# Performance work log

Measured on AMD Instinct MI355X. Metric: run time of the kernel, lower is better.

## Reference

```python
import jax, jax.numpy as jnp
import numpy as np
from jax import lax

ANG = 9
MIND, MAXD = -4, 4
EPS = 1e-5


def conv(x, w, stride=1, dilation=1, padding=0, groups=1):
    return lax.conv_general_dilated(
        x, w, (stride, stride), [(padding, padding)] * 2,
        rhs_dilation=(dilation, dilation),
        dimension_numbers=('NCHW', 'OIHW', 'NCHW'),
        feature_group_count=groups)


def bn_relu(x, g, b):
    # training-mode BatchNorm2d (biased batch stats) + ReLU, as in torch default forward
    m = x.mean((0, 2, 3), keepdims=True)
    v = ((x - m) ** 2).mean((0, 2, 3), keepdims=True)
    y = (x - m) * lax.rsqrt(v + EPS) * g.reshape(1, -1, 1, 1) + b.reshape(1, -1, 1, 1)
    return jax.nn.relu(y)


def sai2macpi(x, ang):
    # out[:, :, i*ang+u, j*ang+v] = x[:, :, u*h+i, v*w+j]  (pure strided rearrange)
    b, c, hu, wv = x.shape
    h, w = hu // ang, wv // ang
    x = x.reshape(b, c, ang, h, ang, w)
    return x.transpose(0, 1, 3, 2, 5, 4).reshape(b, c, h * ang, w * ang)


def _shift_idx(n, ang, dil, pad):
    # per-view-block gather indices replicating Unfold(k=ang,dil,pad,stride=ang)->Fold
    idx = jnp.arange(n)[:, None] * ang + jnp.arange(ang)[None, :] * dil - pad  # [n, ang]
    valid = (idx >= 0) & (idx < n * ang)
    return jnp.clip(idx, 0, n * ang - 1).reshape(-1), valid.reshape(-1)


def disp_shift(feat, d, ang):
    b, c, hu, wv = feat.shape
    h, w = hu // ang, wv // ang
    if d < 0:
        dil = -d * ang + 1
        pad = ang * (ang - 1) * (-d) // 2
    elif d == 0:
        dil, pad = 1, 0
    else:
        dil = d * ang - 1
        pad = ang * (ang - 1) * d // 2 - ang + 1
    ih, mh = _shift_idx(h, ang, dil, pad)
    iw, mw = _shift_idx(w, ang, dil, pad)
    out = feat[:, :, ih, :][:, :, :, iw]
    mask = (mh[:, None] & mw[None, :]).astype(feat.dtype)
    return out * mask


def setup_inputs() -> dict:
    key = jax.random.key(0)
    ks = jax.random.split(key, 16)
    b, h, w = 2, 96, 96
    hu, wv = h * ANG, w * ANG
    s = 0.1
    inp = {
        'x': jax.random.normal(ks[0], (b, 1, hu, wv), jnp.float32),
        'fw0': jax.random.normal(ks[1], (7, 1, 3, 3), jnp.float32) * s,
        'fg0': jnp.ones((7,), jnp.float32),
        'fb0': jnp.zeros((7,), jnp.float32),
        'fw': jax.random.normal(ks[2], (6, 7, 7, 3, 3), jnp.float32) * s,
        'fg': jnp.ones((6, 7), jnp.float32),
        'fb': jnp.zeros((6, 7), jnp.float32),
        'bc_w': jax.random.normal(ks[3], (144, 7, 9, 9), jnp.float32) * 0.04,
        'agg0_dw': jax.random.normal(ks[4], (144, 1, 3, 3), jnp.float32) * s,
        'agg0_dg': jnp.ones((144,), jnp.float32),
        'agg0_db': jnp.zeros((144,), jnp.float32),
        'agg0_pw': jax.random.normal(ks[5], (180, 144, 1, 1), jnp.float32) * s,
        'agg0_pg': jnp.ones((180,), jnp.float32),
        'agg0_pb': jnp.zeros((180,), jnp.float32),
        'aggm_dw': jax.random.normal(ks[6], (4, 180, 1, 3, 3), jnp.float32) * s,
        'aggm_dg': jnp.ones((4, 180), jnp.float32),
        'aggm_db': jnp.zeros((4, 180), jnp.float32),
        'aggm_pw': jax.random.normal(ks[7], (4, 180, 180, 1, 1), jnp.float32) * s,
        'aggm_pg': jnp.ones((4, 180), jnp.float32),
        'aggm_pb': jnp.zeros((4, 180), jnp.float32),
        'last_dw': jax.random.normal(ks[8], (180, 1, 3, 3), jnp.float32) * s,
        'last_dg': jnp.ones((180,), jnp.float32),
        'last_db': jnp.zeros((180,), jnp.float32),
        'last_pw': jax.random.normal(ks[9], (9, 180, 1, 1), jnp.float32) * s,
    }
    return inp


def reference(x, fw0, fg0, fb0, fw, fg, fb, bc_w,
              agg0_dw, agg0_dg, agg0_db, agg0_pw, agg0_pg, agg0_pb,
              aggm_dw, aggm_dg, aggm_db, aggm_pw, aggm_pg, aggm_pb,
              last_dw, last_dg, last_db, last_pw):
    # SAI -> MacPI rearrange
    f = sai2macpi(x, ANG)
    f = bn_relu(conv(f, fw0, dilation=ANG, padding=ANG), fg0, fb0)
    for i in range(6):
        f = bn_relu(conv(f, fw[i], dilation=ANG, padding=ANG), fg[i], fb[i])
    # per-disparity Unfold/Fold shift -> concat [b, 9*7, hu, wv]
    vol = jnp.concatenate([disp_shift(f, d, ANG) for d in range(MIND, MAXD + 1)], axis=1)
    # BuildCost: grouped conv, kernel=stride=angRes -> [b, 144, h, w]
    cv = conv(vol, bc_w, stride=ANG, groups=9)
    # aggregation: depthwise-separable blocks
    y = bn_relu(conv(cv, agg0_dw, padding=1, groups=144), agg0_dg, agg0_db)
    y = bn_relu(conv(y, agg0_pw), agg0_pg, agg0_pb)
    for i in range(4):
        y = bn_relu(conv(y, aggm_dw[i], padding=1, groups=180), aggm_dg[i], aggm_db[i])
        y = bn_relu(conv(y, aggm_pw[i]), aggm_pg[i], aggm_pb[i])
    y = bn_relu(conv(y, last_dw, padding=1, groups=180), last_dg, last_db)
    cost = conv(y, last_pw)  # [b, 9, h, w]
    score = jax.nn.softmax(cost, axis=1)
    disps = jnp.arange(MIND, MAXD + 1, dtype=score.dtype).reshape(1, -1, 1, 1)
    return jnp.sum(score * disps, axis=1, keepdims=True)  # [b, 1, h, w]
```

## Files before the change

kernel.cpp:

```cpp
#include <hip/hip_runtime.h>

#define ANG 9
#define HH 96
#define BB 2
#define PLANE_F (81*HH*HH)
#define PLANE_A (HH*HH)
#define NBLK_FEAT 1458
#define INV_NSMALL (1.0f / 18432.0f)

typedef float f4 __attribute__((ext_vector_type(4), aligned(4)));

__device__ __forceinline__ void row3sel(const float* rp, int base, bool j0, bool j95,
                                        float& w0, float& w1, float& w2) {
  f4 v = *(const f4*)(rp + base);
  w0 = j95 ? v.z : v.x;
  w1 = j0 ? v.x : (j95 ? v.w : v.y);
  w2 = j0 ? v.y : v.z;
}

__global__ __launch_bounds__(256) void k_bnfinal(const float* __restrict__ psum,
    const float* __restrict__ psq, const float* __restrict__ g, const float* __restrict__ bbias,
    float* __restrict__ sc, float* __restrict__ sh, int NB, float invN) {
  int c = blockIdx.x, tid = threadIdx.x;
  float s = 0.f, q = 0.f;
  for (int k = tid; k < NB; k += 256) { s += psum[c * NB + k]; q += psq[c * NB + k]; }
  __shared__ float ss[256], qq[256];
  ss[tid] = s; qq[tid] = q;
  __syncthreads();
  for (int st = 128; st > 0; st >>= 1) {
    if (tid < st) { ss[tid] += ss[tid + st]; qq[tid] += qq[tid + st]; }
    __syncthreads();
  }
  if (tid == 0) {
    float mean = ss[0] * invN;
    float var = fmaxf(qq[0] * invN - mean * mean, 0.f);
    float scale = g[c] / sqrtf(var + 1e-5f);
    sc[c] = scale; sh[c] = bbias[c] - mean * scale;
  }
}

__global__ __launch_bounds__(256) void k_wprep(const float* __restrict__ bcw,
    const float* __restrict__ a0pw, const float* __restrict__ ampw, const float* __restrict__ lpw,
    float* __restrict__ wt, float* __restrict__ wpt) {
  int k = blockIdx.x * 256 + threadIdx.x;
  if (k < 81648) {
    int o = k & 15; int rest = k >> 4;
    int r81 = rest % 81; int gc = rest / 81;
    int c = gc % 7, g = gc / 7;
    wt[k] = bcw[((g * 16 + o) * 7 + c) * 81 + r81];
    return;
  }
  int t = k - 81648;
  if (t < 25920) {
    int c = t / 180, o = t % 180;
    wpt[t] = a0pw[o * 144 + c];
  } else if (t < 25920 + 129600) {
    int t2 = t - 25920;
    int m = t2 / 32400, r = t2 % 32400;
    int c = r / 180, o = r % 180;
    wpt[t] = ampw[m * 32400 + o * 180 + c];
  } else if (t < 25920 + 129600 + 1620) {
    int t2 = t - 25920 - 129600;
    int c = t2 / 9, o = t2 % 9;
    wpt[t] = lpw[o * 180 + c];
  }
}

__global__ __launch_bounds__(256, 4) void k_featconv0(const float* __restrict__ x,
    const float* __restrict__ w, float* __restrict__ out,
    float* __restrict__ psum, float* __restrict__ psq) {
  int blk = blockIdx.x, tid = threadIdx.x;
  int view = blk / 9, q = blk % 9;
  int b = view / 81, uv = view % 81;
  int u = uv / 9, v = uv % 9;
  int widx = q * 256 + tid;
  int j = widx % HH, i0 = (widx / HH) * 4;
  bool j0 = (j == 0), j95 = (j == 95);
  int base = j0 ? 0 : (j95 ? 92 : j - 1);
  float me0 = j0 ? 0.f : 1.f, me2 = j95 ? 0.f : 1.f;
  const float* bx = x + (size_t)b * PLANE_F + (u * HH) * 864 + v * HH;
  float win[6][3];
  #pragma unroll
  for (int r6 = 0; r6 < 6; r6++) {
    int ii = i0 + r6 - 1;
    float mi = ((unsigned)ii < 96u) ? 1.f : 0.f;
    int iic = min(max(ii, 0), 95);
    float w0, w1, w2;
    row3sel(bx + iic * 864, base, j0, j95, w0, w1, w2);
    win[r6][0] = w0 * (mi * me0);
    win[r6][1] = w1 * mi;
    win[r6][2] = w2 * (mi * me2);
  }
  float acc[4][7];
  #pragma unroll
  for (int px = 0; px < 4; px++)
    #pragma unroll
    for (int o = 0; o < 7; o++) acc[px][o] = 0.f;
  #pragma unroll
  for (int o = 0; o < 7; o++) {
    const float* wc = w + o * 9;
    #pragma unroll
    for (int ky = 0; ky < 3; ky++)
      #pragma unroll
      for (int kx = 0; kx < 3; kx++) {
        float wv = wc[ky * 3 + kx];
        #pragma unroll
        for (int px = 0; px < 4; px++)
          acc[px][o] = fmaf(win[px + ky][kx], wv, acc[px][o]);
      }
  }
  #pragma unroll
  for (int o = 0; o < 7; o++) {
    float* op = out + ((size_t)(b * 7 + o)) * PLANE_F + uv * PLANE_A + i0 * HH + j;
    #pragma unroll
    for (int px = 0; px < 4; px++) op[px * HH] = acc[px][o];
  }
  float sv[7], qv[7];
  #pragma unroll
  for (int o = 0; o < 7; o++) {
    sv[o] = acc[0][o] + acc[1][o] + acc[2][o] + acc[3][o];
    qv[o] = acc[0][o]*acc[0][o] + acc[1][o]*acc[1][o] + acc[2][o]*acc[2][o] + acc[3][o]*acc[3][o];
  }
  #pragma unroll
  for (int off2 = 32; off2 > 0; off2 >>= 1)
    #pragma unroll
    for (int o = 0; o < 7; o++) { sv[o] += __shfl_down(sv[o], off2); qv[o] += __shfl_down(qv[o], off2); }
  __shared__ float red[4][14];
  int wave = tid >> 6, lane = tid & 63;
  if (lane == 0) {
    #pragma unroll
    for (int o = 0; o < 7; o++) { red[wave][o] = sv[o]; red[wave][7 + o] = qv[o]; }
  }
  __syncthreads();
  if (tid < 14) {
    float t4 = red[0][tid] + red[1][tid] + red[2][tid] + red[3][tid];
    if (tid < 7) psum[tid * NBLK_FEAT + blk] = t4;
    else         psq[(tid - 7) * NBLK_FEAT + blk] = t4;
  }
}

__global__ __launch_bounds__(256, 4) void k_featconv4(const float* __restrict__ in,
    const float* __restrict__ w, const float* __restrict__ sc, const float* __restrict__ sh,
    float* __restrict__ out, float* __restrict__ psum, float* __restrict__ psq) {
  int blk = blockIdx.x, tid = threadIdx.x;
  int view = blk / 9, q = blk % 9;
  int b = view / 81, uv = view % 81;
  int widx = q * 256 + tid;
  int j = widx % HH, i0 = (widx / HH) * 4;
  bool j0 = (j == 0), j95 = (j == 95);
  int base = j0 ? 0 : (j95 ? 92 : j - 1);
  float me0 = j0 ? 0.f : 1.f, me2 = j95 ? 0.f : 1.f;
  float mrow[6]; int roff[6];
  #pragma unroll
  for (int r6 = 0; r6 < 6; r6++) {
    int ii = i0 + r6 - 1;
    mrow[r6] = ((unsigned)ii < 96u) ? 1.f : 0.f;
    roff[r6] = min(max(ii, 0), 95) * HH + base;
  }
  float acc[4][7];
  #pragma unroll
  for (int px = 0; px < 4; px++)
    #pragma unroll
    for (int o = 0; o < 7; o++) acc[px][o] = 0.f;
  const float* ipbase = in + ((size_t)(b * 7)) * PLANE_F + uv * PLANE_A;
  float pre[6][3];
  #pragma unroll
  for (int r6 = 0; r6 < 6; r6++)
    row3sel(ipbase + roff[r6], 0, j0, j95, pre[r6][0], pre[r6][1], pre[r6][2]);
  #pragma unroll 1
  for (int c = 0; c < 7; c++) {
    float s = sc[c], h2 = sh[c];
    float win[6][3];
    #pragma unroll
    for (int r6 = 0; r6 < 6; r6++) {
      win[r6][0] = fmaxf(fmaf(pre[r6][0], s, h2), 0.f) * (mrow[r6] * me0);
      win[r6][1] = fmaxf(fmaf(pre[r6][1], s, h2), 0.f) * mrow[r6];
      win[r6][2] = fmaxf(fmaf(pre[r6][2], s, h2), 0.f) * (mrow[r6] * me2);
    }
    if (c < 6) {
      const float* ipn = ipbase + (size_t)(c + 1) * PLANE_F;
      #pragma unroll
      for (int r6 = 0; r6 < 6; r6++)
        row3sel(ipn + roff[r6], 0, j0, j95, pre[r6][0], pre[r6][1], pre[r6][2]);
    }
    #pragma unroll
    for (int o = 0; o < 7; o++) {
      const float* wc = w + (o * 7 + c) * 9;
      #pragma unroll
      for (int ky = 0; ky < 3; ky++)
        #pragma unroll
        for (int kx = 0; kx < 3; kx++) {
          float wv = wc[ky * 3 + kx];
          #pragma unroll
          for (int px = 0; px < 4; px++)
            acc[px][o] = fmaf(win[px + ky][kx], wv, acc[px][o]);
        }
    }
  }
  #pragma unroll
  for (int o = 0; o < 7; o++) {
    float* op = out + ((size_t)(b * 7 + o)) * PLANE_F + uv * PLANE_A + i0 * HH + j;
    #pragma unroll
    for (int px = 0; px < 4; px++) op[px * HH] = acc[px][o];
  }
  float sv[7], qv[7];
  #pragma unroll
  for (int o = 0; o < 7; o++) {
    sv[o] = acc[0][o] + acc[1][o] + acc[2][o] + acc[3][o];
    qv[o] = acc[0][o]*acc[0][o] + acc[1][o]*acc[1][o] + acc[2][o]*acc[2][o] + acc[3][o]*acc[3][o];
  }
  #pragma unroll
  for (int off2 = 32; off2 > 0; off2 >>= 1)
    #pragma unroll
    for (int o = 0; o < 7; o++) { sv[o] += __shfl_down(sv[o], off2); qv[o] += __shfl_down(qv[o], off2); }
  __shared__ float red[4][14];
  int wave = tid >> 6, lane = tid & 63;
  if (lane == 0) {
    #pragma unroll
    for (int o = 0; o < 7; o++) { red[wave][o] = sv[o]; red[wave][7 + o] = qv[o]; }
  }
  __syncthreads();
  if (tid < 14) {
    float t4 = red[0][tid] + red[1][tid] + red[2][tid] + red[3][tid];
    if (tid < 7) psum[tid * NBLK_FEAT + blk] = t4;
    else         psq[(tid - 7) * NBLK_FEAT + blk] = t4;
  }
}

__global__ __launch_bounds__(256) void k_buildcost(const float* __restrict__ F,
    const float* __restrict__ sc, const float* __restrict__ sh,
    const float* __restrict__ wt, float* __restrict__ cva, float* __restrict__ cvb) {
  int g = blockIdx.x, tid = threadIdx.x;
  int b = blockIdx.z >> 1, half = blockIdx.z & 1;
  int c0 = half ? 4 : 0;
  int ncu = half ? 27 : 36;
  int d = g - 4;
  bool flip = d > 0;
  int p = blockIdx.y * 256 + tid;
  int i = p / HH, j = p % HH;
  int voff[9]; float mj[9];
  #pragma unroll
  for (int v = 0; v < 9; v++) {
    int jj = j + d * (4 - v);
    mj[v] = ((unsigned)jj < 96u) ? 1.f : 0.f;
    voff[v] = v * PLANE_A + min(max(jj, 0), 95);
  }
  float acc[16];
  #pragma unroll
  for (int o = 0; o < 16; o++) acc[o] = 0.f;
  const float* Fb = F + ((size_t)(b * 7)) * PLANE_F;
  auto LD = [&](int c, int u, float* raw, float& mi) {
    int ii = i + d * (4 - u);
    mi = ((unsigned)ii < 96u) ? 1.f : 0.f;
    int iic = min(max(ii, 0), 95);
    const float* rowb = Fb + (size_t)c * PLANE_F + (u * 9) * PLANE_A + iic * HH;
    #pragma unroll
    for (int v = 0; v < 9; v++) raw[v] = rowb[voff[v]];
  };
  float raw[9], mi_pf;
  LD(c0, 0, raw, mi_pf);
  #pragma unroll 1
  for (int cu = 0; cu < ncu; cu++) {
    int c = c0 + cu / 9, u = cu % 9;
    float cr[9], mi = mi_pf;
    #pragma unroll
    for (int v = 0; v < 9; v++) cr[v] = raw[v];
    if (cu + 1 < ncu) {
      int cn = c0 + (cu + 1) / 9, un = (cu + 1) % 9;
      LD(cn, un, raw, mi_pf);
    }
    float s = sc[c], h2 = sh[c];
    int uw = flip ? 8 - u : u;
    const float* wbase = wt + ((size_t)((g * 7 + c) * 81 + uw * 9)) * 16;
    #pragma unroll
    for (int v = 0; v < 9; v++) {
      float a = fmaxf(fmaf(cr[v], s, h2), 0.f) * (mi * mj[v]);
      int vw = flip ? 8 - v : v;
      const float* wp = wbase + vw * 16;
      #pragma unroll
      for (int o = 0; o < 16; o++) acc[o] = fmaf(wp[o], a, acc[o]);
    }
  }
  float* cv = half ? cvb : cva;
  size_t cvbase = ((size_t)(b * 144 + g * 16)) * PLANE_A + p;
  #pragma unroll
  for (int o = 0; o < 16; o++) cv[cvbase + o * PLANE_A] = acc[o];
}

template<bool AFF, bool SUM2>
__global__ __launch_bounds__(256) void k_dwconv(const float* __restrict__ in,
    const float* __restrict__ in2, const float* __restrict__ w,
    const float* __restrict__ pps, const float* __restrict__ ppq,
    const float* __restrict__ g, const float* __restrict__ bbias,
    float* __restrict__ out, float* __restrict__ dps, float* __restrict__ dpq, int C) {
  int blk = blockIdx.x, tid = threadIdx.x;
  int q = blk % 9; int rr = blk / 9; int c = rr % C; int b = rr / C;
  __shared__ float scsh[2];
  float s = 1.f, h2 = 0.f;
  if (AFF) {
    float si = 0.f, qi = 0.f;
    if (tid < 64) {
      si = pps[c * 72 + tid]; qi = ppq[c * 72 + tid];
      if (tid < 8) { si += pps[c * 72 + 64 + tid]; qi += ppq[c * 72 + 64 + tid]; }
    }
    #pragma unroll
    for (int off = 32; off > 0; off >>= 1) { si += __shfl_down(si, off); qi += __shfl_down(qi, off); }
    if (tid == 0) {
      float mean = si * INV_NSMALL;
      float var = fmaxf(qi * INV_NSMALL - mean * mean, 0.f);
      float scale = g[c] / sqrtf(var + 1e-5f);
      scsh[0] = scale; scsh[1] = bbias[c] - mean * scale;
    }
    __syncthreads();
    s = scsh[0]; h2 = scsh[1];
  }
  int widx = q * 256 + tid;
  int j = widx % HH, i0 = (widx / HH) * 4;
  bool j0 = (j == 0), j95 = (j == 95);
  int base = j0 ? 0 : (j95 ? 92 : j - 1);
  float me0 = j0 ? 0.f : 1.f, me2 = j95 ? 0.f : 1.f;
  const float* wc = w + c * 9;
  const float* ip = in + ((size_t)(b * C + c)) * PLANE_A;
  const float* ip2 = SUM2 ? in2 + ((size_t)(b * C + c)) * PLANE_A : nullptr;
  float win[6][3];
  #pragma unroll
  for (int r6 = 0; r6 < 6; r6++) {
    int ii = i0 + r6 - 1;
    float mi = ((unsigned)ii < 96u) ? 1.f : 0.f;
    int iic = min(max(ii, 0), 95);
    float w0, w1, w2;
    row3sel(ip + iic * HH, base, j0, j95, w0, w1, w2);
    if (SUM2) {
      float x0, x1, x2;
      row3sel(ip2 + iic * HH, base, j0, j95, x0, x1, x2);
      w0 += x0; w1 += x1; w2 += x2;
    }
    if (AFF) {
      w0 = fmaxf(fmaf(w0, s, h2), 0.f);
      w1 = fmaxf(fmaf(w1, s, h2), 0.f);
      w2 = fmaxf(fmaf(w2, s, h2), 0.f);
    }
    win[r6][0] = w0 * (mi * me0);
    win[r6][1] = w1 * mi;
    win[r6][2] = w2 * (mi * me2);
  }
  float acc[4];
  #pragma unroll
  for (int px = 0; px < 4; px++) acc[px] = 0.f;
  #pragma unroll
  for (int ky = 0; ky < 3; ky++)
    #pragma unroll
    for (int kx = 0; kx < 3; kx++) {
      float wv = wc[ky * 3 + kx];
      #pragma unroll
      for (int px = 0; px < 4; px++)
        acc[px] = fmaf(win[px + ky][kx], wv, acc[px]);
    }
  float* op = out + ((size_t)(b * C + c)) * PLANE_A + i0 * HH + j;
  #pragma unroll
  for (int px = 0; px < 4; px++) op[px * HH] = acc[px];
  float sv = acc[0] + acc[1] + acc[2] + acc[3];
  float qv = acc[0]*acc[0] + acc[1]*acc[1] + acc[2]*acc[2] + acc[3]*acc[3];
  #pragma unroll
  for (int off2 = 32; off2 > 0; off2 >>= 1) { sv += __shfl_down(sv, off2); qv += __shfl_down(qv, off2); }
  __shared__ float red[4][2];
  int wave = tid >> 6, lane = tid & 63;
  if (lane == 0) { red[wave][0] = sv; red[wave][1] = qv; }
  __syncthreads();
  if (tid == 0) {
    float S = red[0][0] + red[1][0] + red[2][0] + red[3][0];
    float Q = red[0][1] + red[1][1] + red[2][1] + red[3][1];
    dps[c * 18 + b * 9 + q] = S;
    dpq[c * 18 + b * 9 + q] = Q;
  }
}

template<int K>
__global__ __launch_bounds__(256) void k_pwconv(const float* __restrict__ in,
    const float* __restrict__ dps, const float* __restrict__ dpq,
    const float* __restrict__ g, const float* __restrict__ bbias,
    const float* __restrict__ wpt, float* __restrict__ out,
    float* __restrict__ pps, float* __restrict__ ppq) {
  int tid = threadIdx.x;
  __shared__ float2 scsh[K];
  if (tid < K) {
    float S = 0.f, Q = 0.f;
    #pragma unroll 1
    for (int k = 0; k < 18; k++) { S += dps[tid * 18 + k]; Q += dpq[tid * 18 + k]; }
    float mean = S * INV_NSMALL;
    float var = fmaxf(Q * INV_NSMALL - mean * mean, 0.f);
    float scale = g[tid] / sqrtf(var + 1e-5f);
    scsh[tid] = make_float2(scale, bbias[tid] - mean * scale);
  }
  __syncthreads();
  int posblk = blockIdx.y;
  int p = posblk * 256 + tid;
  int b = p / PLANE_A, pp = p - b * PLANE_A;
  int obase = blockIdx.x * 18;
  float acc[18];
  #pragma unroll
  for (int o = 0; o < 18; o++) acc[o] = 0.f;
  const float* ib = in + (size_t)b * K * PLANE_A + pp;
  float xn[4];
  #pragma unroll
  for (int q2 = 0; q2 < 4; q2++) xn[q2] = ib[(size_t)q2 * PLANE_A];
  #pragma unroll 1
  for (int c0 = 0; c0 < K; c0 += 4) {
    float xv[4];
    #pragma unroll
    for (int q2 = 0; q2 < 4; q2++) xv[q2] = xn[q2];
    if (c0 + 4 < K) {
      #pragma unroll
      for (int q2 = 0; q2 < 4; q2++) xn[q2] = ib[(size_t)(c0 + 4 + q2) * PLANE_A];
    }
    #pragma unroll
    for (int q2 = 0; q2 < 4; q2++) {
      int c = c0 + q2;
      float2 ss = scsh[c];
      float v = fmaxf(fmaf(xv[q2], ss.x, ss.y), 0.f);
      const float* wc = wpt + (size_t)c * 180 + obase;
      #pragma unroll
      for (int o = 0; o < 18; o++)
        acc[o] = fmaf(wc[o], v, acc[o]);
    }
  }
  #pragma unroll
  for (int o = 0; o < 18; o++)
    out[((size_t)(b * 180 + obase + o)) * PLANE_A + pp] = acc[o];
  __shared__ float rs[4][18], rq[4][18];
  int wave = tid >> 6, lane = tid & 63;
  #pragma unroll
  for (int o = 0; o < 18; o++) {
    float s = acc[o], q = acc[o] * acc[o];
    #pragma unroll
    for (int off = 32; off > 0; off >>= 1) { s += __shfl_down(s, off); q += __shfl_down(q, off); }
    if (lane == 0) { rs[wave][o] = s; rq[wave][o] = q; }
  }
  __syncthreads();
  if (tid < 18)
    pps[(obase + tid) * 72 + posblk] = rs[0][tid] + rs[1][tid] + rs[2][tid] + rs[3][tid];
  else if (tid < 36) {
    int o = tid - 18;
    ppq[(obase + o) * 72 + posblk] = rq[0][o] + rq[1][o] + rq[2][o] + rq[3][o];
  }
}

__global__ __launch_bounds__(256) void k_final(const float* __restrict__ in,
    const float* __restrict__ dps, const float* __restrict__ dpq,
    const float* __restrict__ g, const float* __restrict__ bbias,
    const float* __restrict__ wpt, float* __restrict__ out) {
  int tid = threadIdx.x;
  __shared__ float2 scsh[180];
  if (tid < 180) {
    float S = 0.f, Q = 0.f;
    #pragma unroll 1
    for (int k = 0; k < 18; k++) { S += dps[tid * 18 + k]; Q += dpq[tid * 18 + k]; }
    float mean = S * INV_NSMALL;
    float var = fmaxf(Q * INV_NSMALL - mean * mean, 0.f);
    float scale = g[tid] / sqrtf(var + 1e-5f);
    scsh[tid] = make_float2(scale, bbias[tid] - mean * scale);
  }
  __syncthreads();
  int t = blockIdx.x * 256 + tid;
  int b = t / PLANE_A, p = t - b * PLANE_A;
  const float* ib = in + (size_t)b * 180 * PLANE_A + p;
  float acc[9];
  #pragma unroll
  for (int o = 0; o < 9; o++) acc[o] = 0.f;
  float xn[4];
  #pragma unroll
  for (int q2 = 0; q2 < 4; q2++) xn[q2] = ib[(size_t)q2 * PLANE_A];
  #pragma unroll 1
  for (int c0 = 0; c0 < 180; c0 += 4) {
    float xv[4];
    #pragma unroll
    for (int q2 = 0; q2 < 4; q2++) xv[q2] = xn[q2];
    if (c0 + 4 < 180) {
      #pragma unroll
      for (int q2 = 0; q2 < 4; q2++) xn[q2] = ib[(size_t)(c0 + 4 + q2) * PLANE_A];
    }
    #pragma unroll
    for (int q2 = 0; q2 < 4; q2++) {
      int c = c0 + q2;
      float2 ss = scsh[c];
      float v = fmaxf(fmaf(xv[q2], ss.x, ss.y), 0.f);
      const float* wc = wpt + (size_t)c * 9;
      #pragma unroll
      for (int o = 0; o < 9; o++) acc[o] = fmaf(wc[o], v, acc[o]);
    }
  }
  float m = acc[0];
  #pragma unroll
  for (int o = 1; o < 9; o++) m = fmaxf(m, acc[o]);
  float se = 0.f, num = 0.f;
  #pragma unroll
  for (int o = 0; o < 9; o++) {
    float e = expf(acc[o] - m);
    se += e;
    num += (float)(o - 4) * e;
  }
  out[t] = num / se;
}

extern "C" void kernel_launch(void* const* d_in, const int* in_sizes, int n_in,
                              void* d_out, int out_size, void* d_ws, size_t ws_size,
                              hipStream_t stream) {
  const float* x    = (const float*)d_in[0];
  const float* fw0  = (const float*)d_in[1];
  const float* fg0  = (const float*)d_in[2];
  const float* fb0  = (const float*)d_in[3];
  const float* fw   = (const float*)d_in[4];
  const float* fg   = (const float*)d_in[5];
  const float* fb   = (const float*)d_in[6];
  const float* bcw  = (const float*)d_in[7];
  const float* a0dw = (const float*)d_in[8];
  const float* a0dg = (const float*)d_in[9];
  const float* a0db = (const float*)d_in[10];
  const float* a0pw = (const float*)d_in[11];
  const float* a0pg = (const float*)d_in[12];
  const float* a0pb = (const float*)d_in[13];
  const float* amdw = (const float*)d_in[14];
  const float* amdg = (const float*)d_in[15];
  const float* amdb = (const float*)d_in[16];
  const float* ampw = (const float*)d_in[17];
  const float* ampg = (const float*)d_in[18];
  const float* ampb = (const float*)d_in[19];
  const float* ldw  = (const float*)d_in[20];
  const float* ldg  = (const float*)d_in[21];
  const float* ldb  = (const float*)d_in[22];
  const float* lpw  = (const float*)d_in[23];
  float* outp = (float*)d_out;

  float* FA    = (float*)d_ws;
  float* FB    = FA + (size_t)BB * 7 * PLANE_F;
  float* CVA   = FB + (size_t)BB * 7 * PLANE_F;
  float* CVB   = CVA + (size_t)BB * 144 * PLANE_A;
  float* GA    = CVB + (size_t)BB * 144 * PLANE_A;
  float* GB    = GA + (size_t)BB * 180 * PLANE_A;
  float* PSUM  = GB + (size_t)BB * 180 * PLANE_A;
  float* PSQ   = PSUM + 180 * 288;
  float* PPS   = PSQ + 180 * 288;
  float* PPQ   = PPS + 180 * 72;
  float* SC    = PPQ + 180 * 72;
  float* SH    = SC + 180;
  float* WT    = SH + 180;
  float* WPT   = WT + 81648;
  float* WPT_A0 = WPT;
  float* WPT_AM = WPT + 25920;
  float* WPT_L  = WPT + 25920 + 129600;

  const float invNbig = 1.0f / (float)(BB * PLANE_F);

  k_wprep<<<(238788 + 255) / 256, 256, 0, stream>>>(bcw, a0pw, ampw, lpw, WT, WPT);

  k_featconv0<<<NBLK_FEAT, 256, 0, stream>>>(x, fw0, FA, PSUM, PSQ);
  k_bnfinal<<<7, 256, 0, stream>>>(PSUM, PSQ, fg0, fb0, SC, SH, NBLK_FEAT, invNbig);

  float* cur = FA; float* nxt = FB;
  for (int i = 0; i < 6; i++) {
    k_featconv4<<<NBLK_FEAT, 256, 0, stream>>>(cur, fw + i * 441, SC, SH, nxt, PSUM, PSQ);
    k_bnfinal<<<7, 256, 0, stream>>>(PSUM, PSQ, fg + i * 7, fb + i * 7, SC, SH, NBLK_FEAT, invNbig);
    float* tmp = cur; cur = nxt; nxt = tmp;
  }

  k_buildcost<<<dim3(9, 36, 4), 256, 0, stream>>>(cur, SC, SH, WT, CVA, CVB);

  k_dwconv<false, true><<<BB * 144 * 9, 256, 0, stream>>>(CVA, CVB, a0dw,
      nullptr, nullptr, nullptr, nullptr, GA, PSUM, PSQ, 144);
  k_pwconv<144><<<dim3(10, 72), 256, 0, stream>>>(GA, PSUM, PSQ, a0dg, a0db,
      WPT_A0, GB, PPS, PPQ);

  for (int m = 0; m < 4; m++) {
    const float* pg = (m == 0) ? a0pg : ampg + (m - 1) * 180;
    const float* pb = (m == 0) ? a0pb : ampb + (m - 1) * 180;
    k_dwconv<true, false><<<BB * 180 * 9, 256, 0, stream>>>(GB, nullptr, amdw + m * 1620,
        PPS, PPQ, pg, pb, GA, PSUM, PSQ, 180);
    k_pwconv<180><<<dim3(10, 72), 256, 0, stream>>>(GA, PSUM, PSQ,
        amdg + m * 180, amdb + m * 180, WPT_AM + m * 32400, GB, PPS, PPQ);
  }

  k_dwconv<true, false><<<BB * 180 * 9, 256, 0, stream>>>(GB, nullptr, ldw,
      PPS, PPQ, ampg + 540, ampb + 540, GA, PSUM, PSQ, 180);

  k_final<<<72, 256, 0, stream>>>(GA, PSUM, PSQ, ldg, ldb, WPT_L, outp);
}
```

Baseline: 685.9 us.

## Store feature maps channel-interleaved (8-wide) for vectorized loads in feature conv and buildcost

Feature tensors move from planar NCHW to a per-pixel layout that packs the 7 channels plus one pad into 8 floats. The first and subsequent feature convs now write two float4 stores per pixel and read all channels of a neighbour with two vector loads, looping over spatial taps instead of channels. BuildCost reads four channels at once with one float4 load per view instead of one scalar gather per channel. This raises the feature buffers' memory footprint by 8/7 and breaks coalescing across lanes, since adjacent lanes are now 32 bytes apart, in exchange for fewer load instructions.

```diff
diff --git a/kernel.cpp b/kernel.cpp
--- a/kernel.cpp
+++ b/kernel.cpp
@@ -9,6 +9,9 @@
 #define INV_NSMALL (1.0f / 18432.0f)
 
 typedef float f4 __attribute__((ext_vector_type(4), aligned(4)));
+typedef float f4a __attribute__((ext_vector_type(4)));
+
+#define FIDX(b, uv, i, j) ((((size_t)((b) * 81 + (uv))) * PLANE_A + (i) * HH + (j)) * 8)
 
 __device__ __forceinline__ void row3sel(const float* rp, int base, bool j0, bool j95,
                                         float& w0, float& w1, float& w2) {
@@ -110,10 +113,12 @@
       }
   }
   #pragma unroll
-  for (int o = 0; o < 7; o++) {
-    float* op = out + ((size_t)(b * 7 + o)) * PLANE_F + uv * PLANE_A + i0 * HH + j;
-    #pragma unroll
-    for (int px = 0; px < 4; px++) op[px * HH] = acc[px][o];
+  for (int px = 0; px < 4; px++) {
+    float* op = out + FIDX(b, uv, i0 + px, j);
+    f4a s0 = { acc[px][0], acc[px][1], acc[px][2], acc[px][3] };
+    f4a s1 = { acc[px][4], acc[px][5], acc[px][6], 0.f };
+    *(f4a*)(op) = s0;
+    *(f4a*)(op + 4) = s1;
   }
   float sv[7], qv[7];
   #pragma unroll
@@ -148,60 +153,59 @@
   int widx = q * 256 + tid;
   int j = widx % HH, i0 = (widx / HH) * 4;
   bool j0 = (j == 0), j95 = (j == 95);
-  int base = j0 ? 0 : (j95 ? 92 : j - 1);
-  float me0 = j0 ? 0.f : 1.f, me2 = j95 ? 0.f : 1.f;
-  float mrow[6]; int roff[6];
+  float me[3];
+  me[0] = j0 ? 0.f : 1.f; me[1] = 1.f; me[2] = j95 ? 0.f : 1.f;
+  int jc[3];
+  jc[0] = j0 ? j : j - 1; jc[1] = j; jc[2] = j95 ? j : j + 1;
+  float scr[7], shr[7];
+  #pragma unroll
+  for (int c = 0; c < 7; c++) { scr[c] = sc[c]; shr[c] = sh[c]; }
+  float acc[4][7];
+  #pragma unroll
+  for (int px = 0; px < 4; px++)
+    #pragma unroll
+    for (int o = 0; o < 7; o++) acc[px][o] = 0.f;
   #pragma unroll
   for (int r6 = 0; r6 < 6; r6++) {
     int ii = i0 + r6 - 1;
-    mrow[r6] = ((unsigned)ii < 96u) ? 1.f : 0.f;
-    roff[r6] = min(max(ii, 0), 95) * HH + base;
-  }
-  float acc[4][7];
-  #pragma unroll
-  for (int px = 0; px < 4; px++)
-    #pragma unroll
-    for (int o = 0; o < 7; o++) acc[px][o] = 0.f;
-  const float* ipbase = in + ((size_t)(b * 7)) * PLANE_F + uv * PLANE_A;
-  float pre[6][3];
-  #pragma unroll
-  for (int r6 = 0; r6 < 6; r6++)
-    row3sel(ipbase + roff[r6], 0, j0, j95, pre[r6][0], pre[r6][1], pre[r6][2]);
-  #pragma unroll 1
-  for (int c = 0; c < 7; c++) {
-    float s = sc[c], h2 = sh[c];
-    float win[6][3];
-    #pragma unroll
-    for (int r6 = 0; r6 < 6; r6++) {
-      win[r6][0] = fmaxf(fmaf(pre[r6][0], s, h2), 0.f) * (mrow[r6] * me0);
-      win[r6][1] = fmaxf(fmaf(pre[r6][1], s, h2), 0.f) * mrow[r6];
-      win[r6][2] = fmaxf(fmaf(pre[r6][2], s, h2), 0.f) * (mrow[r6] * me2);
-    }
-    if (c < 6) {
-      const float* ipn = ipbase + (size_t)(c + 1) * PLANE_F;
-      #pragma unroll
-      for (int r6 = 0; r6 < 6; r6++)
-        row3sel(ipn + roff[r6], 0, j0, j95, pre[r6][0], pre[r6][1], pre[r6][2]);
-    }
-    #pragma unroll
-    for (int o = 0; o < 7; o++) {
-      const float* wc = w + (o * 7 + c) * 9;
-      #pragma unroll
-      for (int ky = 0; ky < 3; ky++)
-        #pragma unroll
-        for (int kx = 0; kx < 3; kx++) {
-          float wv = wc[ky * 3 + kx];
+    float mi = ((unsigned)ii < 96u) ? 1.f : 0.f;
+    int iic = min(max(ii, 0), 95);
+    #pragma unroll
+    for (int dx = 0; dx < 3; dx++) {
+      const float* pp = in + FIDX(b, uv, iic, jc[dx]);
+      f4a pA = *(const f4a*)(pp);
+      f4a pB = *(const f4a*)(pp + 4);
+      float msk = mi * me[dx];
+      float vals[7];
+      vals[0] = fmaxf(fmaf(pA.x, scr[0], shr[0]), 0.f) * msk;
+      vals[1] = fmaxf(fmaf(pA.y, scr[1], shr[1]), 0.f) * msk;
+      vals[2] = fmaxf(fmaf(pA.z, scr[2], shr[2]), 0.f) * msk;
+      vals[3] = fmaxf(fmaf(pA.w, scr[3], shr[3]), 0.f) * msk;
+      vals[4] = fmaxf(fmaf(pB.x, scr[4], shr[4]), 0.f) * msk;
+      vals[5] = fmaxf(fmaf(pB.y, scr[5], shr[5]), 0.f) * msk;
+      vals[6] = fmaxf(fmaf(pB.z, scr[6], shr[6]), 0.f) * msk;
+      #pragma unroll
+      for (int ky = 0; ky < 3; ky++) {
+        int px = r6 - ky;
+        if (px >= 0 && px < 4) {
           #pragma unroll
-          for (int px = 0; px < 4; px++)
-            acc[px][o] = fmaf(win[px + ky][kx], wv, acc[px][o]);
+          for (int o = 0; o < 7; o++) {
+            const float* wo = w + (o * 7) * 9 + ky * 3 + dx;
+            #pragma unroll
+            for (int c = 0; c < 7; c++)
+              acc[px][o] = fmaf(vals[c], wo[c * 9], acc[px][o]);
+          }
         }
-    }
-  }
-  #pragma unroll
-  for (int o = 0; o < 7; o++) {
-    float* op = out + ((size_t)(b * 7 + o)) * PLANE_F + uv * PLANE_A + i0 * HH + j;
-    #pragma unroll
-    for (int px = 0; px < 4; px++) op[px * HH] = acc[px][o];
+      }
+    }
+  }
+  #pragma unroll
+  for (int px = 0; px < 4; px++) {
+    float* op = out + FIDX(b, uv, i0 + px, j);
+    f4a s0 = { acc[px][0], acc[px][1], acc[px][2], acc[px][3] };
+    f4a s1 = { acc[px][4], acc[px][5], acc[px][6], 0.f };
+    *(f4a*)(op) = s0;
+    *(f4a*)(op + 4) = s1;
   }
   float sv[7], qv[7];
   #pragma unroll
@@ -233,52 +237,54 @@
   int g = blockIdx.x, tid = threadIdx.x;
   int b = blockIdx.z >> 1, half = blockIdx.z & 1;
   int c0 = half ? 4 : 0;
-  int ncu = half ? 27 : 36;
+  int nc = half ? 3 : 4;
   int d = g - 4;
   bool flip = d > 0;
   int p = blockIdx.y * 256 + tid;
   int i = p / HH, j = p % HH;
-  int voff[9]; float mj[9];
+  int jcc[9]; float mj[9];
   #pragma unroll
   for (int v = 0; v < 9; v++) {
     int jj = j + d * (4 - v);
     mj[v] = ((unsigned)jj < 96u) ? 1.f : 0.f;
-    voff[v] = v * PLANE_A + min(max(jj, 0), 95);
+    jcc[v] = min(max(jj, 0), 95);
+  }
+  float scr[4], shr[4];
+  #pragma unroll
+  for (int c = 0; c < 4; c++) {
+    int cc = c0 + (c < nc ? c : 0);
+    scr[c] = sc[cc]; shr[c] = sh[cc];
   }
   float acc[16];
   #pragma unroll
   for (int o = 0; o < 16; o++) acc[o] = 0.f;
-  const float* Fb = F + ((size_t)(b * 7)) * PLANE_F;
-  auto LD = [&](int c, int u, float* raw, float& mi) {
+  #pragma unroll 1
+  for (int u = 0; u < 9; u++) {
     int ii = i + d * (4 - u);
-    mi = ((unsigned)ii < 96u) ? 1.f : 0.f;
+    float mi = ((unsigned)ii < 96u) ? 1.f : 0.f;
     int iic = min(max(ii, 0), 95);
-    const float* rowb = Fb + (size_t)c * PLANE_F + (u * 9) * PLANE_A + iic * HH;
-    #pragma unroll
-    for (int v = 0; v < 9; v++) raw[v] = rowb[voff[v]];
-  };
-  float raw[9], mi_pf;
-  LD(c0, 0, raw, mi_pf);
-  #pragma unroll 1
-  for (int cu = 0; cu < ncu; cu++) {
-    int c = c0 + cu / 9, u = cu % 9;
-    float cr[9], mi = mi_pf;
-    #pragma unroll
-    for (int v = 0; v < 9; v++) cr[v] = raw[v];
-    if (cu + 1 < ncu) {
-      int cn = c0 + (cu + 1) / 9, un = (cu + 1) % 9;
-      LD(cn, un, raw, mi_pf);
-    }
-    float s = sc[c], h2 = sh[c];
     int uw = flip ? 8 - u : u;
-    const float* wbase = wt + ((size_t)((g * 7 + c) * 81 + uw * 9)) * 16;
     #pragma unroll
     for (int v = 0; v < 9; v++) {
-      float a = fmaxf(fmaf(cr[v], s, h2), 0.f) * (mi * mj[v]);
+      const float* pp = F + FIDX(b, u * 9 + v, iic, jcc[v]) + c0;
+      f4a pv = *(const f4a*)(pp);
+      float msk = mi * mj[v];
+      float a0 = fmaxf(fmaf(pv.x, scr[0], shr[0]), 0.f) * msk;
+      float a1 = fmaxf(fmaf(pv.y, scr[1], shr[1]), 0.f) * msk;
+      float a2 = fmaxf(fmaf(pv.z, scr[2], shr[2]), 0.f) * msk;
+      float a3 = fmaxf(fmaf(pv.w, scr[3], shr[3]), 0.f) * msk;
       int vw = flip ? 8 - v : v;
-      const float* wp = wbase + vw * 16;
-      #pragma unroll
-      for (int o = 0; o < 16; o++) acc[o] = fmaf(wp[o], a, acc[o]);
+      const float* wb = wt + ((size_t)((g * 7 + c0) * 81 + uw * 9 + vw)) * 16;
+      #pragma unroll
+      for (int o = 0; o < 16; o++) acc[o] = fmaf(wb[o], a0, acc[o]);
+      #pragma unroll
+      for (int o = 0; o < 16; o++) acc[o] = fmaf(wb[81 * 16 + o], a1, acc[o]);
+      #pragma unroll
+      for (int o = 0; o < 16; o++) acc[o] = fmaf(wb[2 * 81 * 16 + o], a2, acc[o]);
+      if (nc == 4) {
+        #pragma unroll
+        for (int o = 0; o < 16; o++) acc[o] = fmaf(wb[3 * 81 * 16 + o], a3, acc[o]);
+      }
     }
   }
   float* cv = half ? cvb : cva;
@@ -531,9 +537,10 @@
   const float* lpw  = (const float*)d_in[23];
   float* outp = (float*)d_out;
 
+  const size_t FSZ = (size_t)BB * 81 * PLANE_A * 8;
   float* FA    = (float*)d_ws;
-  float* FB    = FA + (size_t)BB * 7 * PLANE_F;
-  float* CVA   = FB + (size_t)BB * 7 * PLANE_F;
+  float* FB    = FA + FSZ;
+  float* CVA   = FB + FSZ;
   float* CVB   = CVA + (size_t)BB * 144 * PLANE_A;
   float* GA    = CVB + (size_t)BB * 144 * PLANE_A;
   float* GB    = GA + (size_t)BB * 180 * PLANE_A;
```

Result: slower. 1.282 ms (+86.9%).
